# Kernel optimization log

Measured on AMD Instinct MI355X. Metric: run time of the kernel, lower is better.

## Reference

```python
import jax, jax.numpy as jnp
import numpy as np

B, S_LONG, S_SHORT, C_IN, H, D_STATE = 16384, 100, 10, 4, 64, 16
BN_EPS = 1e-5


def setup_inputs() -> dict:
    key = jax.random.key(0)
    ks = jax.random.split(key, 32)
    n = lambda i, shape, s=0.1: (jax.random.normal(ks[i], shape, dtype=jnp.float32) * s)
    inp = {
        "x": jax.random.normal(ks[0], (B, S_LONG, C_IN), dtype=jnp.float32),
        # ConvolutionalEyes (Conv1d weights are [out, in, k])
        "conv1_w": n(1, (H, C_IN, 3)), "conv1_b": n(2, (H,)),
        "conv2_w": n(3, (H, H, 5)),    "conv2_b": n(4, (H,)),
        "conv3_w": n(5, (H, H, 7)),    "conv3_b": n(6, (H,)),
        # BatchNorm1d (eval mode: running_mean=0, running_var=1)
        "bn1_g": jnp.ones((H,)), "bn1_b": jnp.zeros((H,)),
        "bn2_g": jnp.ones((H,)), "bn2_b": jnp.zeros((H,)),
        "bn3_g": jnp.ones((H,)), "bn3_b": jnp.zeros((H,)),
        # input_proj
        "proj_w": n(7, (C_IN, H)), "proj_b": n(8, (H,)),
        # MambaBlock (proj_in exists in torch code but is unused in forward)
        "A": n(9, (D_STATE, D_STATE)),
        "Bm": n(10, (H, D_STATE)),
        "Cm": n(11, (D_STATE, H)),
        "out_w": n(12, (H, H)), "out_b": n(13, (H,)),
        # ContextualGate
        "g1_w": n(14, (2 * H, H)), "g1_b": n(15, (H,)),
        "g2_w": n(16, (H, H)),     "g2_b": n(17, (H,)),
        # trading head
        "h1_w": n(18, (H, 32)), "h1_b": n(19, (32,)),
        "h2_w": n(20, (32, 3)), "h2_b": n(21, (3,)),
    }
    return inp


def _conv_bn_relu(x, w, b, g, beta, pad):
    # x: [B, C, L], w: [O, I, K]
    y = jax.lax.conv_general_dilated(x, w, (1,), [(pad, pad)],
                                     dimension_numbers=("NCW", "OIW", "NCW"))
    y = y + b[None, :, None]
    # eval-mode BN with running_mean=0, running_var=1
    y = g[None, :, None] * y * jax.lax.rsqrt(jnp.float32(1.0 + BN_EPS)) + beta[None, :, None]
    return jax.nn.relu(y)


def reference(x, conv1_w, conv1_b, conv2_w, conv2_b, conv3_w, conv3_b,
              bn1_g, bn1_b, bn2_g, bn2_b, bn3_g, bn3_b,
              proj_w, proj_b, A, Bm, Cm, out_w, out_b,
              g1_w, g1_b, g2_w, g2_b, h1_w, h1_b, h2_w, h2_b):
    # --- split windows ---
    x_short = x[:, -S_SHORT:, :]          # [B, 10, 4]
    x_long = x                            # [B, 100, 4]

    # --- ConvolutionalEyes (dropout = identity in eval) ---
    xc = jnp.swapaxes(x_short, 1, 2)      # [B, 4, 10]
    xc = _conv_bn_relu(xc, conv1_w, conv1_b, bn1_g, bn1_b, 1)
    xc = _conv_bn_relu(xc, conv2_w, conv2_b, bn2_g, bn2_b, 2)
    xc = _conv_bn_relu(xc, conv3_w, conv3_b, bn3_g, bn3_b, 3)
    short_features = jnp.mean(xc, axis=2)  # [B, 64]

    # --- input projection ---
    xp = x_long @ proj_w + proj_b          # [B, 100, 64]

    # --- MambaBlock: sequential scan over time ---
    def step(h, x_t):                      # h: [B, 16], x_t: [B, 64]
        h = jnp.tanh(x_t @ Bm + h @ A.T)
        return h, h @ Cm                   # y_t: [B, 64]

    h0 = jnp.zeros((x.shape[0], D_STATE), dtype=x.dtype)
    _, ys = jax.lax.scan(step, h0, jnp.swapaxes(xp, 0, 1))  # ys: [100, B, 64]
    long_context = ys[-1] @ out_w + out_b  # proj_out applied, last timestep

    # --- ContextualGate ---
    combined = jnp.concatenate([short_features, long_context], axis=1)  # [B, 128]
    gate = jax.nn.sigmoid(jnp.tanh(combined @ g1_w + g1_b) @ g2_w + g2_b)
    filtered = short_features * gate

    # --- trading head (dropout = identity in eval) ---
    logits = jax.nn.relu(filtered @ h1_w + h1_b) @ h2_w + h2_b  # [B, 3]
    return logits
```

## Files before the change

### kernel.cpp

```cpp
#include <hip/hip_runtime.h>
#include <cstddef>

#define NB 16384
#define ITER 4
#define TS 720
#define NRNN (NB/128)

typedef __attribute__((ext_vector_type(8))) _Float16 half8;
typedef __attribute__((ext_vector_type(4))) _Float16 half4;
typedef __attribute__((ext_vector_type(4))) float f32x4;
typedef __attribute__((ext_vector_type(2))) float f32x2;
typedef __attribute__((ext_vector_type(16))) float f32x16;

#define OFF_W1T 0
#define OFF_SC1 768
#define OFF_SH1 832
#define OFF_SC2 896
#define OFF_SH2 960
#define OFF_SC3 1024
#define OFF_SH3 1088
#define OFF_PB  1152
#define OFF_PBB 1216
#define OFF_W2H 2304
#define OFF_W2L 12544
#define OFF_W3H 22784
#define OFF_W3L 37120
#define OFF_SF  51456
#define OFF_H   (51456 + NB*64)
#define OFF_TF  1362176
#define OFF_A2  1378048
#define WS_NEED ((size_t)11863808 * 4)

#define G1H 0
#define G1L 8192
#define G2H 16384
#define G2L 20480
#define H1H 24576
#define H1L 26624
#define H2H 28672
#define H2L 29184
#define COH 29696
#define COL 30720
#define TFH 31744

static __device__ __forceinline__ f32x16 mfma32(half8 a, half8 b, f32x16 c) {
  return __builtin_amdgcn_mfma_f32_32x32x16_f16(a, b, c, 0, 0, 0);
}
static __device__ __forceinline__ f32x4 mfma16(half4 a, half4 b, f32x4 c) {
  return __builtin_amdgcn_mfma_f32_16x16x16f16(a, b, c, 0, 0, 0);
}
static __device__ __forceinline__ f32x4 mfma16k32(half8 a, half8 b, f32x4 c) {
  return __builtin_amdgcn_mfma_f32_16x16x32_f16(a, b, c, 0, 0, 0);
}

__global__ __launch_bounds__(256) void prep_kernel(
    const float* __restrict__ conv1_w, const float* __restrict__ conv1_b,
    const float* __restrict__ conv2_w, const float* __restrict__ conv2_b,
    const float* __restrict__ conv3_w, const float* __restrict__ conv3_b,
    const float* __restrict__ bn1_g, const float* __restrict__ bn1_b,
    const float* __restrict__ bn2_g, const float* __restrict__ bn2_b,
    const float* __restrict__ bn3_g, const float* __restrict__ bn3_b,
    const float* __restrict__ proj_w, const float* __restrict__ proj_b,
    const float* __restrict__ A, const float* __restrict__ Bm,
    const float* __restrict__ Cm, const float* __restrict__ out_w,
    const float* __restrict__ g1_w, const float* __restrict__ g2_w,
    const float* __restrict__ h1_w, const float* __restrict__ h2_w,
    float* __restrict__ ws)
{
  int tid = blockIdx.x * blockDim.x + threadIdx.x;
  int nt = gridDim.x * blockDim.x;
  const float s = rsqrtf(1.0f + 1e-5f);

  for (int i = tid; i < 64*12; i += nt) {
    int o = i & 63, rk = i >> 6;
    ws[OFF_W1T + i] = conv1_w[o*12 + rk];
  }
  for (int o = tid; o < 64; o += nt) {
    float s1 = bn1_g[o]*s, s2 = bn2_g[o]*s, s3 = bn3_g[o]*s;
    ws[OFF_SC1+o] = s1; ws[OFF_SH1+o] = s1*conv1_b[o] + bn1_b[o];
    ws[OFF_SC2+o] = s2; ws[OFF_SH2+o] = s2*conv2_b[o] + bn2_b[o];
    ws[OFF_SC3+o] = s3; ws[OFF_SH3+o] = s3*conv3_b[o] + bn3_b[o];
  }
  {
    _Float16* w2h = (_Float16*)(ws + OFF_W2H);
    _Float16* w2l = (_Float16*)(ws + OFF_W2L);
    for (int i = tid; i < 20*2*64; i += nt) {
      int lane = i & 63, ot = (i >> 6) & 1, sk = i >> 7;
      int tap = sk >> 2, ic0 = (sk & 3)*16 + (lane >> 5)*8;
      int o = ot*32 + (lane & 31);
      #pragma unroll
      for (int j = 0; j < 8; ++j) {
        float w = conv2_w[o*320 + (ic0 + j)*5 + tap];
        _Float16 hi = (_Float16)w;
        w2h[(size_t)i*8 + j] = hi;
        w2l[(size_t)i*8 + j] = (_Float16)(w - (float)hi);
      }
    }
  }
  {
    _Float16* w3h = (_Float16*)(ws + OFF_W3H);
    _Float16* w3l = (_Float16*)(ws + OFF_W3L);
    for (int i = tid; i < 28*2*64; i += nt) {
      int lane = i & 63, ot = (i >> 6) & 1, sk = i >> 7;
      int tap = sk >> 2, ic0 = (sk & 3)*16 + (lane >> 5)*8;
      int o = ot*32 + (lane & 31);
      #pragma unroll
      for (int j = 0; j < 8; ++j) {
        float w = conv3_w[o*448 + (ic0 + j)*7 + tap];
        _Float16 hi = (_Float16)w;
        w3h[(size_t)i*8 + j] = hi;
        w3l[(size_t)i*8 + j] = (_Float16)(w - (float)hi);
      }
    }
  }
  for (int i = tid; i < 64; i += nt) {
    int c = i >> 4, j = i & 15;
    float acc = 0.f;
    for (int m = 0; m < 64; ++m) acc += proj_w[c*64+m]*Bm[m*16+j];
    ws[OFF_PB + i] = acc;
  }
  for (int j = tid; j < 16; j += nt) {
    float acc = 0.f;
    for (int m = 0; m < 64; ++m) acc += proj_b[m]*Bm[m*16+j];
    ws[OFF_PBB + j] = acc;
  }

  _Float16* tf = (_Float16*)(ws + OFF_TF);
  for (int i = tid; i < 16*64; i += nt) {
    int l = i & 63, f = i >> 6, mt = f >> 2, ks = f & 3;
    int o = mt*16 + (l & 15), kb = ks*32 + (l >> 4)*8;
    #pragma unroll
    for (int j = 0; j < 8; ++j) {
      float w = g1_w[(size_t)(kb + j)*64 + o];
      _Float16 hi = (_Float16)w;
      tf[G1H + (size_t)i*8 + j] = hi;
      tf[G1L + (size_t)i*8 + j] = (_Float16)(w - (float)hi);
    }
  }
  for (int i = tid; i < 8*64; i += nt) {
    int l = i & 63, f = i >> 6, mt = f >> 1, ks = f & 1;
    int o = mt*16 + (l & 15), kb = ks*32 + (l >> 4)*8;
    #pragma unroll
    for (int j = 0; j < 8; ++j) {
      float w = g2_w[(size_t)(kb + j)*64 + o];
      _Float16 hi = (_Float16)w;
      tf[G2H + (size_t)i*8 + j] = hi;
      tf[G2L + (size_t)i*8 + j] = (_Float16)(w - (float)hi);
    }
  }
  for (int i = tid; i < 4*64; i += nt) {
    int l = i & 63, f = i >> 6, mt = f >> 1, ks = f & 1;
    int hx = mt*16 + (l & 15), kb = ks*32 + (l >> 4)*8;
    #pragma unroll
    for (int j = 0; j < 8; ++j) {
      float w = h1_w[(size_t)(kb + j)*32 + hx];
      _Float16 hi = (_Float16)w;
      tf[H1H + (size_t)i*8 + j] = hi;
      tf[H1L + (size_t)i*8 + j] = (_Float16)(w - (float)hi);
    }
  }
  for (int i = tid; i < 64; i += nt) {
    int l = i, m = l & 15, kb = (l >> 4)*8;
    #pragma unroll
    for (int j = 0; j < 8; ++j) {
      float w = (m < 3) ? h2_w[(size_t)(kb + j)*3 + m] : 0.f;
      _Float16 hi = (_Float16)w;
      tf[H2H + (size_t)i*8 + j] = hi;
      tf[H2L + (size_t)i*8 + j] = (_Float16)(w - (float)hi);
    }
  }
  for (int i = tid; i < 4*64; i += nt) {
    int l = i & 63, mt = i >> 6;
    int o = mt*16 + (l & 15), kb = (l >> 4)*4;
    #pragma unroll
    for (int j = 0; j < 4; ++j) {
      float acc = 0.f;
      for (int m = 0; m < 64; ++m) acc += Cm[(kb + j)*64 + m]*out_w[m*64 + o];
      _Float16 hi = (_Float16)acc;
      tf[COH + (size_t)i*4 + j] = hi;
      tf[COL + (size_t)i*4 + j] = (_Float16)(acc - (float)hi);
    }
  }
}

__global__ __launch_bounds__(512) void conv12_kernel(
    const float* __restrict__ x, const float* __restrict__ wsr,
    _Float16* __restrict__ a2gh, _Float16* __restrict__ a2gl,
    const float* __restrict__ A, float* __restrict__ hout)
{
  __shared__ __align__(16) _Float16 sW[40960];
  __shared__ __align__(16) _Float16 a1h[16][TS], a1l[16][TS];

  const int tid = threadIdx.x;
  const int lane = tid & 63;
  const int wid = tid >> 6;

  if (blockIdx.x < NRNN) {
    const int colb = lane & 15;
    const int q = lane >> 4;
    const size_t b = ((size_t)blockIdx.x*8 + wid)*16 + colb;

    const f32x4 av = *(const f32x4*)(A + (size_t)(lane & 15)*16 + q*4);
    half4 Ahi, Alo;
    #pragma unroll
    for (int j = 0; j < 4; ++j) {
      _Float16 hi = (_Float16)av[j];
      Ahi[j] = hi;
      Alo[j] = (_Float16)(av[j] - (float)hi);
    }
    f32x4 pb0 = *(const f32x4*)(wsr + OFF_PB + 0*16 + q*4);
    f32x4 pb1 = *(const f32x4*)(wsr + OFF_PB + 1*16 + q*4);
    f32x4 pb2 = *(const f32x4*)(wsr + OFF_PB + 2*16 + q*4);
    f32x4 pb3 = *(const f32x4*)(wsr + OFF_PB + 3*16 + q*4);
    f32x4 pbb = *(const f32x4*)(wsr + OFF_PBB + q*4);

    const float* xb = x + b*400;
    half4 hh = {}, hl = {};
    f32x4 hf;
    #pragma unroll 2
    for (int t = 0; t < 100; ++t) {
      const f32x4 xv = *(const f32x4*)(xb + t*4);
      f32x4 U;
      #pragma unroll
      for (int r = 0; r < 4; ++r)
        U[r] = pbb[r] + xv[0]*pb0[r] + xv[1]*pb1[r] + xv[2]*pb2[r] + xv[3]*pb3[r];
      f32x4 u = mfma16(Alo, hh, U);
      u = mfma16(Ahi, hl, u);
      u = mfma16(Ahi, hh, u);
      #pragma unroll
      for (int r = 0; r < 4; ++r) {
        float e = __expf(2.f*u[r]);
        float hn = 1.f - 2.f/(e + 1.f);
        hf[r] = hn;
        _Float16 hi = (_Float16)hn;
        hh[r] = hi;
        hl[r] = (_Float16)(hn - (float)hi);
      }
    }
    *(f32x4*)(hout + b*16 + q*4) = hf;
    return;
  }

  const int n = lane & 15;
  const int nc = (n < 10) ? n : 9;
  const int kh8 = (lane >> 5) * 8;
  const int rq = 4 * (lane >> 5);
  const int lbL = 2*wid + ((lane >> 4) & 1);
  const half8 z8 = {};
  const size_t B0g = (size_t)(blockIdx.x - NRNN) * 16;

  {
    const f32x4* src = (const f32x4*)(wsr + OFF_W2H);
    f32x4* dst = (f32x4*)sW;
    for (int i = tid; i < 5120; i += 512) dst[i] = src[i];
  }
  {
    const float sc1 = wsr[OFF_SC1 + lane], sh1 = wsr[OFF_SH1 + lane];
    #pragma unroll
    for (int bb = 0; bb < 2; ++bb) {
      const int lb = 2*wid + bb;
      const size_t gb = B0g + lb;
      float xv[4][12];
      #pragma unroll
      for (int c = 0; c < 4; ++c) { xv[c][0] = 0.f; xv[c][11] = 0.f; }
      #pragma unroll
      for (int tt = 0; tt < 10; ++tt)
        #pragma unroll
        for (int c = 0; c < 4; ++c)
          xv[c][1 + tt] = x[gb*400 + (90 + tt)*4 + c];
      float a1[10];
      #pragma unroll
      for (int t = 0; t < 10; ++t) a1[t] = 0.f;
      #pragma unroll
      for (int c = 0; c < 4; ++c)
        #pragma unroll
        for (int k = 0; k < 3; ++k) {
          const float wv = wsr[OFF_W1T + (c*3 + k)*64 + lane];
          #pragma unroll
          for (int t = 0; t < 10; ++t) a1[t] += wv * xv[c][t + k];
        }
      #pragma unroll
      for (int t = 0; t < 10; ++t) {
        float v = sc1*a1[t] + sh1;
        v = v > 0.f ? v : 0.f;
        _Float16 hi = (_Float16)v;
        a1h[lb][t*72 + lane] = hi;
        a1l[lb][t*72 + lane] = (_Float16)(v - (float)hi);
      }
    }
  }
  __syncthreads();

  {
    f32x16 acc0, acc1;
    #pragma unroll
    for (int r = 0; r < 16; ++r) { acc0[r] = 0.f; acc1[r] = 0.f; }
    const _Float16* bhp = &a1h[lbL][0];
    const _Float16* blp = &a1l[lbL][0];
    #pragma unroll
    for (int sk = 0; sk < 20; ++sk) {
      const int tap = sk >> 2, icb = (sk & 3)*16;
      const int t = nc + tap - 2;
      const int tc = t < 0 ? 0 : (t > 9 ? 9 : t);
      const bool valid = (t >= 0) & (t <= 9);
      const int off = tc*72 + icb + kh8;
      half8 bh = *(const half8*)(bhp + off);
      half8 bl = *(const half8*)(blp + off);
      bh = valid ? bh : z8;
      bl = valid ? bl : z8;
      const half8 wh0 = *(const half8*)(sW + (size_t)(sk*2 + 0)*512 + lane*8);
      const half8 wh1 = *(const half8*)(sW + (size_t)(sk*2 + 1)*512 + lane*8);
      const half8 wl0 = *(const half8*)(sW + (size_t)(40 + sk*2)*512 + lane*8);
      const half8 wl1 = *(const half8*)(sW + (size_t)(41 + sk*2)*512 + lane*8);
      acc0 = mfma32(wh0, bh, acc0);
      acc0 = mfma32(wh0, bl, acc0);
      acc0 = mfma32(wl0, bh, acc0);
      acc1 = mfma32(wh1, bh, acc1);
      acc1 = mfma32(wh1, bl, acc1);
      acc1 = mfma32(wl1, bh, acc1);
    }
    if (n < 10) {
      const size_t gb = B0g + lbL;
      auto epi = [&](const f32x16& ac, int ot) {
        #pragma unroll
        for (int q = 0; q < 4; ++q) {
          const int rowb = 8*q + rq + ot*32;
          const f32x4 sc = *(const f32x4*)(wsr + OFF_SC2 + rowb);
          const f32x4 sh = *(const f32x4*)(wsr + OFF_SH2 + rowb);
          half4 h4, l4;
          #pragma unroll
          for (int r = 0; r < 4; ++r) {
            float v = sc[r]*ac[4*q + r] + sh[r];
            v = v > 0.f ? v : 0.f;
            _Float16 hi = (_Float16)v;
            h4[r] = hi;
            l4[r] = (_Float16)(v - (float)hi);
          }
          *(half4*)(a2gh + gb*640 + n*64 + rowb) = h4;
          *(half4*)(a2gl + gb*640 + n*64 + rowb) = l4;
        }
      };
      epi(acc0, 0);
      epi(acc1, 1);
    }
  }
}

__global__ __launch_bounds__(512) void conv3k_kernel(
    const float* __restrict__ wsr,
    const _Float16* __restrict__ a2gh, const _Float16* __restrict__ a2gl,
    float* __restrict__ sfp)
{
  __shared__ __align__(16) _Float16 sW[57344];
  __shared__ __align__(16) _Float16 a2h[16][TS], a2l[16][TS];

  const int tid = threadIdx.x;
  const int lane = tid & 63;
  const int wid = tid >> 6;
  const int n = lane & 15;
  const int nc = (n < 10) ? n : 9;
  const int kh8 = (lane >> 5) * 8;
  const int rq = 4 * (lane >> 5);
  const int lbL = 2*wid + ((lane >> 4) & 1);
  const half8 z8 = {};
  const size_t B0g = (size_t)blockIdx.x * 16;

  {
    const f32x4* src = (const f32x4*)(wsr + OFF_W3H);
    f32x4* dst = (f32x4*)sW;
    for (int i = tid; i < 7168; i += 512) dst[i] = src[i];
  }
  {
    for (int i = tid; i < 1280; i += 512) {
      int idx = i*8;
      int lb = idx / 640, rem = idx % 640;
      int t = rem >> 6, o = rem & 63;
      *(half8*)(&a2h[lb][t*72 + o]) = *(const half8*)(a2gh + (B0g + lb)*640 + rem);
      *(half8*)(&a2l[lb][t*72 + o]) = *(const half8*)(a2gl + (B0g + lb)*640 + rem);
    }
  }
  __syncthreads();

  {
    f32x16 acc0, acc1;
    #pragma unroll
    for (int r = 0; r < 16; ++r) { acc0[r] = 0.f; acc1[r] = 0.f; }
    const _Float16* bhp = &a2h[lbL][0];
    const _Float16* blp = &a2l[lbL][0];
    #pragma unroll
    for (int sk = 0; sk < 28; ++sk) {
      const int tap = sk >> 2, icb = (sk & 3)*16;
      const int t = nc + tap - 3;
      const int tc = t < 0 ? 0 : (t > 9 ? 9 : t);
      const bool valid = (t >= 0) & (t <= 9);
      const int off = tc*72 + icb + kh8;
      half8 bh = *(const half8*)(bhp + off);
      half8 bl = *(const half8*)(blp + off);
      bh = valid ? bh : z8;
      bl = valid ? bl : z8;
      const half8 wh0 = *(const half8*)(sW + (size_t)(sk*2 + 0)*512 + lane*8);
      const half8 wh1 = *(const half8*)(sW + (size_t)(sk*2 + 1)*512 + lane*8);
      const half8 wl0 = *(const half8*)(sW + (size_t)(56 + sk*2)*512 + lane*8);
      const half8 wl1 = *(const half8*)(sW + (size_t)(57 + sk*2)*512 + lane*8);
      acc0 = mfma32(wh0, bh, acc0);
      acc0 = mfma32(wh0, bl, acc0);
      acc0 = mfma32(wl0, bh, acc0);
      acc1 = mfma32(wh1, bh, acc1);
      acc1 = mfma32(wh1, bl, acc1);
      acc1 = mfma32(wl1, bh, acc1);
    }
    auto epi = [&](const f32x16& ac, int ot) {
      #pragma unroll
      for (int q = 0; q < 4; ++q) {
        const int rowb = 8*q + rq + ot*32;
        const f32x4 sc = *(const f32x4*)(wsr + OFF_SC3 + rowb);
        const f32x4 sh = *(const f32x4*)(wsr + OFF_SH3 + rowb);
        f32x4 v;
        #pragma unroll
        for (int r = 0; r < 4; ++r) {
          float t2 = sc[r]*ac[4*q + r] + sh[r];
          t2 = t2 > 0.f ? t2 : 0.f;
          v[r] = (n < 10) ? t2 : 0.f;
        }
        #pragma unroll
        for (int r = 0; r < 4; ++r) {
          v[r] += __shfl_xor(v[r], 1, 16);
          v[r] += __shfl_xor(v[r], 2, 16);
          v[r] += __shfl_xor(v[r], 4, 16);
          v[r] += __shfl_xor(v[r], 8, 16);
        }
        if (n == 0)
          *(f32x4*)(sfp + (B0g + lbL)*64 + rowb) = v * 0.1f;
      }
    };
    epi(acc0, 0);
    epi(acc1, 1);
  }
}

__global__ __launch_bounds__(256) void conv_kernel(
    const float* __restrict__ x, const float* __restrict__ wsr,
    float* __restrict__ sfp)
{
  __shared__ __align__(16) _Float16 sW[57344];
  __shared__ __align__(16) _Float16 a1h[8][TS], a1l[8][TS];
  __shared__ __align__(16) _Float16 a2h[8][TS], a2l[8][TS];

  const int tid = threadIdx.x;
  const int lane = tid & 63;
  const int wid = tid >> 6;
  const int n = lane & 15;
  const int nc = (n < 10) ? n : 9;
  const int kh8 = (lane >> 5) * 8;
  const int rq = 4 * (lane >> 5);
  const int lb0 = (wid >> 1)*4 + (wid & 1)*2;
  const int lbL = lb0 + ((lane >> 4) & 1);
  const half8 z8 = {};
  const float sc1 = wsr[OFF_SC1 + lane], sh1 = wsr[OFF_SH1 + lane];

  for (int it = 0; it < ITER; ++it) {
    const size_t gbase = (size_t)blockIdx.x*(8*ITER) + (size_t)it*8;
    {
      const f32x4* src = (const f32x4*)(wsr + OFF_W2H);
      f32x4* dst = (f32x4*)sW;
      for (int i = tid; i < 5120; i += 256) dst[i] = src[i];
    }
    #pragma unroll
    for (int bb = 0; bb < 2; ++bb) {
      const int lb = lb0 + bb;
      const size_t gb = gbase + lb;
      float xv[4][12];
      #pragma unroll
      for (int c = 0; c < 4; ++c) { xv[c][0] = 0.f; xv[c][11] = 0.f; }
      #pragma unroll
      for (int tt = 0; tt < 10; ++tt)
        #pragma unroll
        for (int c = 0; c < 4; ++c)
          xv[c][1 + tt] = x[gb*400 + (90 + tt)*4 + c];
      float a1[10];
      #pragma unroll
      for (int t = 0; t < 10; ++t) a1[t] = 0.f;
      #pragma unroll
      for (int c = 0; c < 4; ++c)
        #pragma unroll
        for (int k = 0; k < 3; ++k) {
          const float wv = wsr[OFF_W1T + (c*3 + k)*64 + lane];
          #pragma unroll
          for (int t = 0; t < 10; ++t) a1[t] += wv * xv[c][t + k];
        }
      #pragma unroll
      for (int t = 0; t < 10; ++t) {
        float v = sc1*a1[t] + sh1;
        v = v > 0.f ? v : 0.f;
        _Float16 hi = (_Float16)v;
        a1h[lb][t*72 + lane] = hi;
        a1l[lb][t*72 + lane] = (_Float16)(v - (float)hi);
      }
    }
    __syncthreads();
    {
      f32x16 acc0, acc1;
      #pragma unroll
      for (int r = 0; r < 16; ++r) { acc0[r] = 0.f; acc1[r] = 0.f; }
      const _Float16* bhp = &a1h[lbL][0];
      const _Float16* blp = &a1l[lbL][0];
      #pragma unroll
      for (int sk = 0; sk < 20; ++sk) {
        const int tap = sk >> 2, icb = (sk & 3)*16;
        const int t = nc + tap - 2;
        const int tc = t < 0 ? 0 : (t > 9 ? 9 : t);
        const bool valid = (t >= 0) & (t <= 9);
        const int off = tc*72 + icb + kh8;
        half8 bh = *(const half8*)(bhp + off);
        half8 bl = *(const half8*)(blp + off);
        bh = valid ? bh : z8;
        bl = valid ? bl : z8;
        const half8 wh0 = *(const half8*)(sW + (size_t)(sk*2 + 0)*512 + lane*8);
        const half8 wh1 = *(const half8*)(sW + (size_t)(sk*2 + 1)*512 + lane*8);
        const half8 wl0 = *(const half8*)(sW + (size_t)(40 + sk*2)*512 + lane*8);
        const half8 wl1 = *(const half8*)(sW + (size_t)(41 + sk*2)*512 + lane*8);
        acc0 = mfma32(wh0, bh, acc0);
        acc0 = mfma32(wh0, bl, acc0);
        acc0 = mfma32(wl0, bh, acc0);
        acc1 = mfma32(wh1, bh, acc1);
        acc1 = mfma32(wh1, bl, acc1);
        acc1 = mfma32(wl1, bh, acc1);
      }
      if (n < 10) {
        auto epi = [&](const f32x16& ac, int ot) {
          #pragma unroll
          for (int q = 0; q < 4; ++q) {
            const int rowb = 8*q + rq + ot*32;
            const f32x4 sc = *(const f32x4*)(wsr + OFF_SC2 + rowb);
            const f32x4 sh = *(const f32x4*)(wsr + OFF_SH2 + rowb);
            half4 h4, l4;
            #pragma unroll
            for (int r = 0; r < 4; ++r) {
              float v = sc[r]*ac[4*q + r] + sh[r];
              v = v > 0.f ? v : 0.f;
              _Float16 hi = (_Float16)v;
              h4[r] = hi;
              l4[r] = (_Float16)(v - (float)hi);
            }
            *(half4*)(&a2h[lbL][n*72 + rowb]) = h4;
            *(half4*)(&a2l[lbL][n*72 + rowb]) = l4;
          }
        };
        epi(acc0, 0);
        epi(acc1, 1);
      }
    }
    __syncthreads();
    {
      const f32x4* src = (const f32x4*)(wsr + OFF_W3H);
      f32x4* dst = (f32x4*)sW;
      for (int i = tid; i < 7168; i += 256) dst[i] = src[i];
    }
    __syncthreads();
    {
      f32x16 acc0, acc1;
      #pragma unroll
      for (int r = 0; r < 16; ++r) { acc0[r] = 0.f; acc1[r] = 0.f; }
      const _Float16* bhp = &a2h[lbL][0];
      const _Float16* blp = &a2l[lbL][0];
      #pragma unroll
      for (int sk = 0; sk < 28; ++sk) {
        const int tap = sk >> 2, icb = (sk & 3)*16;
        const int t = nc + tap - 3;
        const int tc = t < 0 ? 0 : (t > 9 ? 9 : t);
        const bool valid = (t >= 0) & (t <= 9);
        const int off = tc*72 + icb + kh8;
        half8 bh = *(const half8*)(bhp + off);
        half8 bl = *(const half8*)(blp + off);
        bh = valid ? bh : z8;
        bl = valid ? bl : z8;
        const half8 wh0 = *(const half8*)(sW + (size_t)(sk*2 + 0)*512 + lane*8);
        const half8 wh1 = *(const half8*)(sW + (size_t)(sk*2 + 1)*512 + lane*8);
        const half8 wl0 = *(const half8*)(sW + (size_t)(56 + sk*2)*512 + lane*8);
        const half8 wl1 = *(const half8*)(sW + (size_t)(57 + sk*2)*512 + lane*8);
        acc0 = mfma32(wh0, bh, acc0);
        acc0 = mfma32(wh0, bl, acc0);
        acc0 = mfma32(wl0, bh, acc0);
        acc1 = mfma32(wh1, bh, acc1);
        acc1 = mfma32(wh1, bl, acc1);
        acc1 = mfma32(wl1, bh, acc1);
      }
      auto epi = [&](const f32x16& ac, int ot) {
        #pragma unroll
        for (int q = 0; q < 4; ++q) {
          const int rowb = 8*q + rq + ot*32;
          const f32x4 sc = *(const f32x4*)(wsr + OFF_SC3 + rowb);
          const f32x4 sh = *(const f32x4*)(wsr + OFF_SH3 + rowb);
          f32x4 v;
          #pragma unroll
          for (int r = 0; r < 4; ++r) {
            float t2 = sc[r]*ac[4*q + r] + sh[r];
            t2 = t2 > 0.f ? t2 : 0.f;
            v[r] = (n < 10) ? t2 : 0.f;
          }
          #pragma unroll
          for (int r = 0; r < 4; ++r) {
            v[r] += __shfl_xor(v[r], 1, 16);
            v[r] += __shfl_xor(v[r], 2, 16);
            v[r] += __shfl_xor(v[r], 4, 16);
            v[r] += __shfl_xor(v[r], 8, 16);
          }
          if (n == 0)
            *(f32x4*)(sfp + (gbase + lbL)*64 + rowb) = v * 0.1f;
        }
      };
      epi(acc0, 0);
      epi(acc1, 1);
    }
    __syncthreads();
  }
}

__global__ __launch_bounds__(256) void rnn_kernel(
    const float* __restrict__ x, const float* __restrict__ wsr,
    const float* __restrict__ A, float* __restrict__ hout)
{
  const int lane = threadIdx.x & 63;
  const int wid = threadIdx.x >> 6;
  const int colb = lane & 15;
  const int q = lane >> 4;
  const size_t b = ((size_t)blockIdx.x*4 + wid)*16 + colb;

  const f32x4 av = *(const f32x4*)(A + (size_t)(lane & 15)*16 + q*4);
  half4 Ahi, Alo;
  #pragma unroll
  for (int j = 0; j < 4; ++j) {
    _Float16 hi = (_Float16)av[j];
    Ahi[j] = hi;
    Alo[j] = (_Float16)(av[j] - (float)hi);
  }
  f32x4 pb0 = *(const f32x4*)(wsr + OFF_PB + 0*16 + q*4);
  f32x4 pb1 = *(const f32x4*)(wsr + OFF_PB + 1*16 + q*4);
  f32x4 pb2 = *(const f32x4*)(wsr + OFF_PB + 2*16 + q*4);
  f32x4 pb3 = *(const f32x4*)(wsr + OFF_PB + 3*16 + q*4);
  f32x4 pbb = *(const f32x4*)(wsr + OFF_PBB + q*4);

  const float* xb = x + b*400;
  half4 hh = {}, hl = {};
  f32x4 hf;
  #pragma unroll 2
  for (int t = 0; t < 100; ++t) {
    const f32x4 xv = *(const f32x4*)(xb + t*4);
    f32x4 U;
    #pragma unroll
    for (int r = 0; r < 4; ++r)
      U[r] = pbb[r] + xv[0]*pb0[r] + xv[1]*pb1[r] + xv[2]*pb2[r] + xv[3]*pb3[r];
    f32x4 u = mfma16(Alo, hh, U);
    u = mfma16(Ahi, hl, u);
    u = mfma16(Ahi, hh, u);
    #pragma unroll
    for (int r = 0; r < 4; ++r) {
      float e = __expf(2.f*u[r]);
      float hn = 1.f - 2.f/(e + 1.f);
      hf[r] = hn;
      _Float16 hi = (_Float16)hn;
      hh[r] = hi;
      hl[r] = (_Float16)(hn - (float)hi);
    }
  }
  *(f32x4*)(hout + b*16 + q*4) = hf;
}

#define CMBH 0
#define CMBL 2176
#define T1H  4352
#define T1L  5504
#define FLH  6656
#define FLL  7808
#define RH   8960
#define RL   9600
__global__ __launch_bounds__(256) void tail_kernel(
    const float* __restrict__ wsr,
    const float* __restrict__ g1_b, const float* __restrict__ g2_b,
    const float* __restrict__ h1_b, const float* __restrict__ h2_b,
    const float* __restrict__ out_b, float* __restrict__ out)
{
  __shared__ __align__(16) _Float16 sWF[TFH];
  __shared__ __align__(16) _Float16 sAct[4*10240];

  const int tid = threadIdx.x;
  const int lane = tid & 63;
  const int wid = tid >> 6;
  const int n = lane & 15;
  const int q = lane >> 4;
  const int B0 = blockIdx.x*64 + wid*16;

  {
    const f32x4* src = (const f32x4*)(wsr + OFF_TF);
    f32x4* dst = (f32x4*)sWF;
    for (int i = tid; i < TFH/8; i += 256) dst[i] = src[i];
  }
  __syncthreads();

  _Float16* wa = sAct + wid*10240;
  const float* sf = wsr + OFF_SF;
  const float* hws = wsr + OFF_H;

  const f32x4 hv = *(const f32x4*)(hws + (size_t)(B0 + n)*16 + q*4);
  half4 hh, hl;
  #pragma unroll
  for (int j = 0; j < 4; ++j) {
    _Float16 hi = (_Float16)hv[j];
    hh[j] = hi;
    hl[j] = (_Float16)(hv[j] - (float)hi);
  }
  f32x4 lc[4];
  #pragma unroll
  for (int mt = 0; mt < 4; ++mt) {
    lc[mt] = *(const f32x4*)(out_b + mt*16 + q*4);
    const half4 ah = *(const half4*)(sWF + COH + (size_t)(mt*64 + lane)*4);
    const half4 al = *(const half4*)(sWF + COL + (size_t)(mt*64 + lane)*4);
    lc[mt] = mfma16(al, hh, lc[mt]);
    lc[mt] = mfma16(ah, hl, lc[mt]);
    lc[mt] = mfma16(ah, hh, lc[mt]);
  }
  f32x4 sfv[4];
  #pragma unroll
  for (int mt = 0; mt < 4; ++mt) {
    sfv[mt] = *(const f32x4*)(sf + (size_t)(B0 + n)*64 + mt*16 + q*4);
    half4 sh4, sl4, lh4, ll4;
    #pragma unroll
    for (int r = 0; r < 4; ++r) {
      _Float16 hi = (_Float16)sfv[mt][r];
      sh4[r] = hi; sl4[r] = (_Float16)(sfv[mt][r] - (float)hi);
      _Float16 hi2 = (_Float16)lc[mt][r];
      lh4[r] = hi2; ll4[r] = (_Float16)(lc[mt][r] - (float)hi2);
    }
    *(half4*)(wa + CMBH + n*136 + mt*16 + q*4) = sh4;
    *(half4*)(wa + CMBL + n*136 + mt*16 + q*4) = sl4;
    *(half4*)(wa + CMBH + n*136 + 64 + mt*16 + q*4) = lh4;
    *(half4*)(wa + CMBL + n*136 + 64 + mt*16 + q*4) = ll4;
  }
  f32x4 u1[4];
  #pragma unroll
  for (int mt = 0; mt < 4; ++mt) u1[mt] = *(const f32x4*)(g1_b + mt*16 + q*4);
  #pragma unroll
  for (int ks = 0; ks < 4; ++ks) {
    const half8 bh = *(const half8*)(wa + CMBH + n*136 + ks*32 + q*8);
    const half8 bl = *(const half8*)(wa + CMBL + n*136 + ks*32 + q*8);
    #pragma unroll
    for (int mt = 0; mt < 4; ++mt) {
      const half8 ah = *(const half8*)(sWF + G1H + (size_t)((mt*4 + ks)*64 + lane)*8);
      const half8 al = *(const half8*)(sWF + G1L + (size_t)((mt*4 + ks)*64 + lane)*8);
      u1[mt] = mfma16k32(al, bh, u1[mt]);
      u1[mt] = mfma16k32(ah, bl, u1[mt]);
      u1[mt] = mfma16k32(ah, bh, u1[mt]);
    }
  }
  #pragma unroll
  for (int mt = 0; mt < 4; ++mt) {
    half4 th4, tl4;
    #pragma unroll
    for (int r = 0; r < 4; ++r) {
      float e = __expf(2.f*u1[mt][r]);
      float t1 = 1.f - 2.f/(e + 1.f);
      _Float16 hi = (_Float16)t1;
      th4[r] = hi; tl4[r] = (_Float16)(t1 - (float)hi);
    }
    *(half4*)(wa + T1H + n*72 + mt*16 + q*4) = th4;
    *(half4*)(wa + T1L + n*72 + mt*16 + q*4) = tl4;
  }
  f32x4 u2[4];
  #pragma unroll
  for (int mt = 0; mt < 4; ++mt) u2[mt] = *(const f32x4*)(g2_b + mt*16 + q*4);
  #pragma unroll
  for (int ks = 0; ks < 2; ++ks) {
    const half8 bh = *(const half8*)(wa + T1H + n*72 + ks*32 + q*8);
    const half8 bl = *(const half8*)(wa + T1L + n*72 + ks*32 + q*8);
    #pragma unroll
    for (int mt = 0; mt < 4; ++mt) {
      const half8 ah = *(const half8*)(sWF + G2H + (size_t)((mt*2 + ks)*64 + lane)*8);
      const half8 al = *(const half8*)(sWF + G2L + (size_t)((mt*2 + ks)*64 + lane)*8);
      u2[mt] = mfma16k32(al, bh, u2[mt]);
      u2[mt] = mfma16k32(ah, bl, u2[mt]);
      u2[mt] = mfma16k32(ah, bh, u2[mt]);
    }
  }
  #pragma unroll
  for (int mt = 0; mt < 4; ++mt) {
    half4 fh4, fl4;
    #pragma unroll
    for (int r = 0; r < 4; ++r) {
      float gate = 1.f/(1.f + __expf(-u2[mt][r]));
      float f = sfv[mt][r] * gate;
      _Float16 hi = (_Float16)f;
      fh4[r] = hi; fl4[r] = (_Float16)(f - (float)hi);
    }
    *(half4*)(wa + FLH + n*72 + mt*16 + q*4) = fh4;
    *(half4*)(wa + FLL + n*72 + mt*16 + q*4) = fl4;
  }
  f32x4 u3[2];
  #pragma unroll
  for (int mt = 0; mt < 2; ++mt) u3[mt] = *(const f32x4*)(h1_b + mt*16 + q*4);
  #pragma unroll
  for (int ks = 0; ks < 2; ++ks) {
    const half8 bh = *(const half8*)(wa + FLH + n*72 + ks*32 + q*8);
    const half8 bl = *(const half8*)(wa + FLL + n*72 + ks*32 + q*8);
    #pragma unroll
    for (int mt = 0; mt < 2; ++mt) {
      const half8 ah = *(const half8*)(sWF + H1H + (size_t)((mt*2 + ks)*64 + lane)*8);
      const half8 al = *(const half8*)(sWF + H1L + (size_t)((mt*2 + ks)*64 + lane)*8);
      u3[mt] = mfma16k32(al, bh, u3[mt]);
      u3[mt] = mfma16k32(ah, bl, u3[mt]);
      u3[mt] = mfma16k32(ah, bh, u3[mt]);
    }
  }
  #pragma unroll
  for (int mt = 0; mt < 2; ++mt) {
    half4 rh4, rl4;
    #pragma unroll
    for (int r = 0; r < 4; ++r) {
      float v = fmaxf(u3[mt][r], 0.f);
      _Float16 hi = (_Float16)v;
      rh4[r] = hi; rl4[r] = (_Float16)(v - (float)hi);
    }
    *(half4*)(wa + RH + n*40 + mt*16 + q*4) = rh4;
    *(half4*)(wa + RL + n*40 + mt*16 + q*4) = rl4;
  }
  {
    f32x4 u4;
    if (q == 0) { u4[0] = h2_b[0]; u4[1] = h2_b[1]; u4[2] = h2_b[2]; u4[3] = 0.f; }
    else { u4[0] = 0.f; u4[1] = 0.f; u4[2] = 0.f; u4[3] = 0.f; }
    const half8 bh = *(const half8*)(wa + RH + n*40 + q*8);
    const half8 bl = *(const half8*)(wa + RL + n*40 + q*8);
    const half8 ah = *(const half8*)(sWF + H2H + (size_t)lane*8);
    const half8 al = *(const half8*)(sWF + H2L + (size_t)lane*8);
    u4 = mfma16k32(al, bh, u4);
    u4 = mfma16k32(ah, bl, u4);
    u4 = mfma16k32(ah, bh, u4);
    if (q == 0) {
      out[(size_t)(B0 + n)*3 + 0] = u4[0];
      out[(size_t)(B0 + n)*3 + 1] = u4[1];
      out[(size_t)(B0 + n)*3 + 2] = u4[2];
    }
  }
}

extern "C" void kernel_launch(void* const* d_in, const int* in_sizes, int n_in,
                              void* d_out, int out_size, void* d_ws, size_t ws_size,
                              hipStream_t stream) {
  const float* x       = (const float*)d_in[0];
  const float* conv1_w = (const float*)d_in[1];
  const float* conv1_b = (const float*)d_in[2];
  const float* conv2_w = (const float*)d_in[3];
  const float* conv2_b = (const float*)d_in[4];
  const float* conv3_w = (const float*)d_in[5];
  const float* conv3_b = (const float*)d_in[6];
  const float* bn1_g   = (const float*)d_in[7];
  const float* bn1_b   = (const float*)d_in[8];
  const float* bn2_g   = (const float*)d_in[9];
  const float* bn2_b   = (const float*)d_in[10];
  const float* bn3_g   = (const float*)d_in[11];
  const float* bn3_b   = (const float*)d_in[12];
  const float* proj_w  = (const float*)d_in[13];
  const float* proj_b  = (const float*)d_in[14];
  const float* A       = (const float*)d_in[15];
  const float* Bm      = (const float*)d_in[16];
  const float* Cm      = (const float*)d_in[17];
  const float* out_w   = (const float*)d_in[18];
  const float* out_b   = (const float*)d_in[19];
  const float* g1_w    = (const float*)d_in[20];
  const float* g1_b    = (const float*)d_in[21];
  const float* g2_w    = (const float*)d_in[22];
  const float* g2_b    = (const float*)d_in[23];
  const float* h1_w    = (const float*)d_in[24];
  const float* h1_b    = (const float*)d_in[25];
  const float* h2_w    = (const float*)d_in[26];
  const float* h2_b    = (const float*)d_in[27];
  float* ws = (float*)d_ws;
  float* out = (float*)d_out;

  prep_kernel<<<64, 256, 0, stream>>>(conv1_w, conv1_b, conv2_w, conv2_b,
      conv3_w, conv3_b, bn1_g, bn1_b, bn2_g, bn2_b, bn3_g, bn3_b,
      proj_w, proj_b, A, Bm, Cm, out_w, g1_w, g2_w, h1_w, h2_w, ws);

  if (ws_size >= WS_NEED) {
    _Float16* a2gh = (_Float16*)(ws + OFF_A2);
    _Float16* a2gl = a2gh + (size_t)NB*640;
    conv12_kernel<<<NRNN + NB/16, 512, 0, stream>>>(x, ws, a2gh, a2gl,
        A, ws + OFF_H);
    conv3k_kernel<<<NB/16, 512, 0, stream>>>(ws, a2gh, a2gl, ws + OFF_SF);
  } else {
    conv_kernel<<<NB/(8*ITER), 256, 0, stream>>>(x, ws, ws + OFF_SF);
    rnn_kernel<<<NB/64, 256, 0, stream>>>(x, ws, A, ws + OFF_H);
  }
  tail_kernel<<<NB/64, 256, 0, stream>>>(ws, g1_b, g2_b, h1_b, h2_b, out_b, out);
}
```

Measured before the change: 262.1 us.

## Fuse conv2 and conv3 into one kernel keeping activations in LDS

Merges the conv1/conv2 kernel and the separate conv3 kernel into one kernel. The conv2 output now stays in shared memory and is reused in place for conv3, which removes the fp16 hi/lo activation round trip through global memory and one launch. Both conv stages now read their weights straight from global memory (cached) instead of staging them in LDS. That shrinks the shared-memory footprint and, together with launch_bounds(512,4), is meant to raise occupancy. The trade-off is more global and L2 weight traffic per wave. The fallback conv/rnn path and its workspace check are removed.

```diff
diff --git a/kernel.cpp b/kernel.cpp
--- a/kernel.cpp
+++ b/kernel.cpp
@@ -2,7 +2,6 @@
 #include <cstddef>
 
 #define NB 16384
-#define ITER 4
 #define TS 720
 #define NRNN (NB/128)
 
@@ -28,8 +27,6 @@
 #define OFF_SF  51456
 #define OFF_H   (51456 + NB*64)
 #define OFF_TF  1362176
-#define OFF_A2  1378048
-#define WS_NEED ((size_t)11863808 * 4)
 
 #define G1H 0
 #define G1L 8192
@@ -183,13 +180,12 @@
   }
 }
 
-__global__ __launch_bounds__(512) void conv12_kernel(
+__global__ __launch_bounds__(512, 4) void conv123_kernel(
     const float* __restrict__ x, const float* __restrict__ wsr,
-    _Float16* __restrict__ a2gh, _Float16* __restrict__ a2gl,
-    const float* __restrict__ A, float* __restrict__ hout)
+    const float* __restrict__ A, float* __restrict__ hout,
+    float* __restrict__ sfp)
 {
-  __shared__ __align__(16) _Float16 sW[40960];
-  __shared__ __align__(16) _Float16 a1h[16][TS], a1l[16][TS];
+  __shared__ __align__(16) _Float16 ah[16][TS], al[16][TS];
 
   const int tid = threadIdx.x;
   const int lane = tid & 63;
@@ -250,11 +246,6 @@
   const size_t B0g = (size_t)(blockIdx.x - NRNN) * 16;
 
   {
-    const f32x4* src = (const f32x4*)(wsr + OFF_W2H);
-    f32x4* dst = (f32x4*)sW;
-    for (int i = tid; i < 5120; i += 512) dst[i] = src[i];
-  }
-  {
     const float sc1 = wsr[OFF_SC1 + lane], sh1 = wsr[OFF_SH1 + lane];
     #pragma unroll
     for (int bb = 0; bb < 2; ++bb) {
@@ -284,19 +275,21 @@
         float v = sc1*a1[t] + sh1;
         v = v > 0.f ? v : 0.f;
         _Float16 hi = (_Float16)v;
-        a1h[lb][t*72 + lane] = hi;
-        a1l[lb][t*72 + lane] = (_Float16)(v - (float)hi);
+        ah[lb][t*72 + lane] = hi;
+        al[lb][t*72 + lane] = (_Float16)(v - (float)hi);
       }
     }
   }
-  __syncthreads();
+
+  const _Float16* bhp = &ah[lbL][0];
+  const _Float16* blp = &al[lbL][0];
 
   {
+    const _Float16* w2h = (const _Float16*)(wsr + OFF_W2H);
+    const _Float16* w2l = (const _Float16*)(wsr + OFF_W2L);
     f32x16 acc0, acc1;
     #pragma unroll
     for (int r = 0; r < 16; ++r) { acc0[r] = 0.f; acc1[r] = 0.f; }
-    const _Float16* bhp = &a1h[lbL][0];
-    const _Float16* blp = &a1l[lbL][0];
     #pragma unroll
     for (int sk = 0; sk < 20; ++sk) {
       const int tap = sk >> 2, icb = (sk & 3)*16;
@@ -308,10 +301,10 @@
       half8 bl = *(const half8*)(blp + off);
       bh = valid ? bh : z8;
       bl = valid ? bl : z8;
-      const half8 wh0 = *(const half8*)(sW + (size_t)(sk*2 + 0)*512 + lane*8);
-      const half8 wh1 = *(const half8*)(sW + (size_t)(sk*2 + 1)*512 + lane*8);
-      const half8 wl0 = *(const half8*)(sW + (size_t)(40 + sk*2)*512 + lane*8);
-      const half8 wl1 = *(const half8*)(sW + (size_t)(41 + sk*2)*512 + lane*8);
+      const half8 wh0 = *(const half8*)(w2h + (size_t)(sk*2 + 0)*512 + lane*8);
+      const half8 wh1 = *(const half8*)(w2h + (size_t)(sk*2 + 1)*512 + lane*8);
+      const half8 wl0 = *(const half8*)(w2l + (size_t)(sk*2 + 0)*512 + lane*8);
+      const half8 wl1 = *(const half8*)(w2l + (size_t)(sk*2 + 1)*512 + lane*8);
       acc0 = mfma32(wh0, bh, acc0);
       acc0 = mfma32(wh0, bl, acc0);
       acc0 = mfma32(wl0, bh, acc0);
@@ -320,7 +313,6 @@
       acc1 = mfma32(wl1, bh, acc1);
     }
     if (n < 10) {
-      const size_t gb = B0g + lbL;
       auto epi = [&](const f32x16& ac, int ot) {
         #pragma unroll
         for (int q = 0; q < 4; ++q) {
@@ -336,57 +328,21 @@
             h4[r] = hi;
             l4[r] = (_Float16)(v - (float)hi);
           }
-          *(half4*)(a2gh + gb*640 + n*64 + rowb) = h4;
-          *(half4*)(a2gl + gb*640 + n*64 + rowb) = l4;
+          *(half4*)(&ah[lbL][n*72 + rowb]) = h4;
+          *(half4*)(&al[lbL][n*72 + rowb]) = l4;
         }
       };
       epi(acc0, 0);
       epi(acc1, 1);
     }
   }
-}
-
-__global__ __launch_bounds__(512) void conv3k_kernel(
-    const float* __restrict__ wsr,
-    const _Float16* __restrict__ a2gh, const _Float16* __restrict__ a2gl,
-    float* __restrict__ sfp)
-{
-  __shared__ __align__(16) _Float16 sW[57344];
-  __shared__ __align__(16) _Float16 a2h[16][TS], a2l[16][TS];
-
-  const int tid = threadIdx.x;
-  const int lane = tid & 63;
-  const int wid = tid >> 6;
-  const int n = lane & 15;
-  const int nc = (n < 10) ? n : 9;
-  const int kh8 = (lane >> 5) * 8;
-  const int rq = 4 * (lane >> 5);
-  const int lbL = 2*wid + ((lane >> 4) & 1);
-  const half8 z8 = {};
-  const size_t B0g = (size_t)blockIdx.x * 16;
 
   {
-    const f32x4* src = (const f32x4*)(wsr + OFF_W3H);
-    f32x4* dst = (f32x4*)sW;
-    for (int i = tid; i < 7168; i += 512) dst[i] = src[i];
-  }
-  {
-    for (int i = tid; i < 1280; i += 512) {
-      int idx = i*8;
-      int lb = idx / 640, rem = idx % 640;
-      int t = rem >> 6, o = rem & 63;
-      *(half8*)(&a2h[lb][t*72 + o]) = *(const half8*)(a2gh + (B0g + lb)*640 + rem);
-      *(half8*)(&a2l[lb][t*72 + o]) = *(const half8*)(a2gl + (B0g + lb)*640 + rem);
-    }
-  }
-  __syncthreads();
-
-  {
+    const _Float16* w3h = (const _Float16*)(wsr + OFF_W3H);
+    const _Float16* w3l = (const _Float16*)(wsr + OFF_W3L);
     f32x16 acc0, acc1;
     #pragma unroll
     for (int r = 0; r < 16; ++r) { acc0[r] = 0.f; acc1[r] = 0.f; }
-    const _Float16* bhp = &a2h[lbL][0];
-    const _Float16* blp = &a2l[lbL][0];
     #pragma unroll
     for (int sk = 0; sk < 28; ++sk) {
       const int tap = sk >> 2, icb = (sk & 3)*16;
@@ -398,10 +354,10 @@
       half8 bl = *(const half8*)(blp + off);
       bh = valid ? bh : z8;
       bl = valid ? bl : z8;
-      const half8 wh0 = *(const half8*)(sW + (size_t)(sk*2 + 0)*512 + lane*8);
-      const half8 wh1 = *(const half8*)(sW + (size_t)(sk*2 + 1)*512 + lane*8);
-      const half8 wl0 = *(const half8*)(sW + (size_t)(56 + sk*2)*512 + lane*8);
-      const half8 wl1 = *(const half8*)(sW + (size_t)(57 + sk*2)*512 + lane*8);
+      const half8 wh0 = *(const half8*)(w3h + (size_t)(sk*2 + 0)*512 + lane*8);
+      const half8 wh1 = *(const half8*)(w3h + (size_t)(sk*2 + 1)*512 + lane*8);
+      const half8 wl0 = *(const half8*)(w3l + (size_t)(sk*2 + 0)*512 + lane*8);
+      const half8 wl1 = *(const half8*)(w3l + (size_t)(sk*2 + 1)*512 + lane*8);
       acc0 = mfma32(wh0, bh, acc0);
       acc0 = mfma32(wh0, bl, acc0);
       acc0 = mfma32(wl0, bh, acc0);
@@ -436,234 +392,6 @@
     epi(acc0, 0);
     epi(acc1, 1);
   }
-}
-
-__global__ __launch_bounds__(256) void conv_kernel(
-    const float* __restrict__ x, const float* __restrict__ wsr,
-    float* __restrict__ sfp)
-{
-  __shared__ __align__(16) _Float16 sW[57344];
-  __shared__ __align__(16) _Float16 a1h[8][TS], a1l[8][TS];
-  __shared__ __align__(16) _Float16 a2h[8][TS], a2l[8][TS];
-
-  const int tid = threadIdx.x;
-  const int lane = tid & 63;
-  const int wid = tid >> 6;
-  const int n = lane & 15;
-  const int nc = (n < 10) ? n : 9;
-  const int kh8 = (lane >> 5) * 8;
-  const int rq = 4 * (lane >> 5);
-  const int lb0 = (wid >> 1)*4 + (wid & 1)*2;
-  const int lbL = lb0 + ((lane >> 4) & 1);
-  const half8 z8 = {};
-  const float sc1 = wsr[OFF_SC1 + lane], sh1 = wsr[OFF_SH1 + lane];
-
-  for (int it = 0; it < ITER; ++it) {
-    const size_t gbase = (size_t)blockIdx.x*(8*ITER) + (size_t)it*8;
-    {
-      const f32x4* src = (const f32x4*)(wsr + OFF_W2H);
-      f32x4* dst = (f32x4*)sW;
-      for (int i = tid; i < 5120; i += 256) dst[i] = src[i];
-    }
-    #pragma unroll
-    for (int bb = 0; bb < 2; ++bb) {
-      const int lb = lb0 + bb;
-      const size_t gb = gbase + lb;
-      float xv[4][12];
-      #pragma unroll
-      for (int c = 0; c < 4; ++c) { xv[c][0] = 0.f; xv[c][11] = 0.f; }
-      #pragma unroll
-      for (int tt = 0; tt < 10; ++tt)
-        #pragma unroll
-        for (int c = 0; c < 4; ++c)
-          xv[c][1 + tt] = x[gb*400 + (90 + tt)*4 + c];
-      float a1[10];
-      #pragma unroll
-      for (int t = 0; t < 10; ++t) a1[t] = 0.f;
-      #pragma unroll
-      for (int c = 0; c < 4; ++c)
-        #pragma unroll
-        for (int k = 0; k < 3; ++k) {
-          const float wv = wsr[OFF_W1T + (c*3 + k)*64 + lane];
-          #pragma unroll
-          for (int t = 0; t < 10; ++t) a1[t] += wv * xv[c][t + k];
-        }
-      #pragma unroll
-      for (int t = 0; t < 10; ++t) {
-        float v = sc1*a1[t] + sh1;
-        v = v > 0.f ? v : 0.f;
-        _Float16 hi = (_Float16)v;
-        a1h[lb][t*72 + lane] = hi;
-        a1l[lb][t*72 + lane] = (_Float16)(v - (float)hi);
-      }
-    }
-    __syncthreads();
-    {
-      f32x16 acc0, acc1;
-      #pragma unroll
-      for (int r = 0; r < 16; ++r) { acc0[r] = 0.f; acc1[r] = 0.f; }
-      const _Float16* bhp = &a1h[lbL][0];
-      const _Float16* blp = &a1l[lbL][0];
-      #pragma unroll
-      for (int sk = 0; sk < 20; ++sk) {
-        const int tap = sk >> 2, icb = (sk & 3)*16;
-        const int t = nc + tap - 2;
-        const int tc = t < 0 ? 0 : (t > 9 ? 9 : t);
-        const bool valid = (t >= 0) & (t <= 9);
-        const int off = tc*72 + icb + kh8;
-        half8 bh = *(const half8*)(bhp + off);
-        half8 bl = *(const half8*)(blp + off);
-        bh = valid ? bh : z8;
-        bl = valid ? bl : z8;
-        const half8 wh0 = *(const half8*)(sW + (size_t)(sk*2 + 0)*512 + lane*8);
-        const half8 wh1 = *(const half8*)(sW + (size_t)(sk*2 + 1)*512 + lane*8);
-        const half8 wl0 = *(const half8*)(sW + (size_t)(40 + sk*2)*512 + lane*8);
-        const half8 wl1 = *(const half8*)(sW + (size_t)(41 + sk*2)*512 + lane*8);
-        acc0 = mfma32(wh0, bh, acc0);
-        acc0 = mfma32(wh0, bl, acc0);
-        acc0 = mfma32(wl0, bh, acc0);
-        acc1 = mfma32(wh1, bh, acc1);
-        acc1 = mfma32(wh1, bl, acc1);
-        acc1 = mfma32(wl1, bh, acc1);
-      }
-      if (n < 10) {
-        auto epi = [&](const f32x16& ac, int ot) {
-          #pragma unroll
-          for (int q = 0; q < 4; ++q) {
-            const int rowb = 8*q + rq + ot*32;
-            const f32x4 sc = *(const f32x4*)(wsr + OFF_SC2 + rowb);
-            const f32x4 sh = *(const f32x4*)(wsr + OFF_SH2 + rowb);
-            half4 h4, l4;
-            #pragma unroll
-            for (int r = 0; r < 4; ++r) {
-              float v = sc[r]*ac[4*q + r] + sh[r];
-              v = v > 0.f ? v : 0.f;
-              _Float16 hi = (_Float16)v;
-              h4[r] = hi;
-              l4[r] = (_Float16)(v - (float)hi);
-            }
-            *(half4*)(&a2h[lbL][n*72 + rowb]) = h4;
-            *(half4*)(&a2l[lbL][n*72 + rowb]) = l4;
-          }
-        };
-        epi(acc0, 0);
-        epi(acc1, 1);
-      }
-    }
-    __syncthreads();
-    {
-      const f32x4* src = (const f32x4*)(wsr + OFF_W3H);
-      f32x4* dst = (f32x4*)sW;
-      for (int i = tid; i < 7168; i += 256) dst[i] = src[i];
-    }
-    __syncthreads();
-    {
-      f32x16 acc0, acc1;
-      #pragma unroll
-      for (int r = 0; r < 16; ++r) { acc0[r] = 0.f; acc1[r] = 0.f; }
-      const _Float16* bhp = &a2h[lbL][0];
-      const _Float16* blp = &a2l[lbL][0];
-      #pragma unroll
-      for (int sk = 0; sk < 28; ++sk) {
-        const int tap = sk >> 2, icb = (sk & 3)*16;
-        const int t = nc + tap - 3;
-        const int tc = t < 0 ? 0 : (t > 9 ? 9 : t);
-        const bool valid = (t >= 0) & (t <= 9);
-        const int off = tc*72 + icb + kh8;
-        half8 bh = *(const half8*)(bhp + off);
-        half8 bl = *(const half8*)(blp + off);
-        bh = valid ? bh : z8;
-        bl = valid ? bl : z8;
-        const half8 wh0 = *(const half8*)(sW + (size_t)(sk*2 + 0)*512 + lane*8);
-        const half8 wh1 = *(const half8*)(sW + (size_t)(sk*2 + 1)*512 + lane*8);
-        const half8 wl0 = *(const half8*)(sW + (size_t)(56 + sk*2)*512 + lane*8);
-        const half8 wl1 = *(const half8*)(sW + (size_t)(57 + sk*2)*512 + lane*8);
-        acc0 = mfma32(wh0, bh, acc0);
-        acc0 = mfma32(wh0, bl, acc0);
-        acc0 = mfma32(wl0, bh, acc0);
-        acc1 = mfma32(wh1, bh, acc1);
-        acc1 = mfma32(wh1, bl, acc1);
-        acc1 = mfma32(wl1, bh, acc1);
-      }
-      auto epi = [&](const f32x16& ac, int ot) {
-        #pragma unroll
-        for (int q = 0; q < 4; ++q) {
-          const int rowb = 8*q + rq + ot*32;
-          const f32x4 sc = *(const f32x4*)(wsr + OFF_SC3 + rowb);
-          const f32x4 sh = *(const f32x4*)(wsr + OFF_SH3 + rowb);
-          f32x4 v;
-          #pragma unroll
-          for (int r = 0; r < 4; ++r) {
-            float t2 = sc[r]*ac[4*q + r] + sh[r];
-            t2 = t2 > 0.f ? t2 : 0.f;
-            v[r] = (n < 10) ? t2 : 0.f;
-          }
-          #pragma unroll
-          for (int r = 0; r < 4; ++r) {
-            v[r] += __shfl_xor(v[r], 1, 16);
-            v[r] += __shfl_xor(v[r], 2, 16);
-            v[r] += __shfl_xor(v[r], 4, 16);
-            v[r] += __shfl_xor(v[r], 8, 16);
-          }
-          if (n == 0)
-            *(f32x4*)(sfp + (gbase + lbL)*64 + rowb) = v * 0.1f;
-        }
-      };
-      epi(acc0, 0);
-      epi(acc1, 1);
-    }
-    __syncthreads();
-  }
-}
-
-__global__ __launch_bounds__(256) void rnn_kernel(
-    const float* __restrict__ x, const float* __restrict__ wsr,
-    const float* __restrict__ A, float* __restrict__ hout)
-{
-  const int lane = threadIdx.x & 63;
-  const int wid = threadIdx.x >> 6;
-  const int colb = lane & 15;
-  const int q = lane >> 4;
-  const size_t b = ((size_t)blockIdx.x*4 + wid)*16 + colb;
-
-  const f32x4 av = *(const f32x4*)(A + (size_t)(lane & 15)*16 + q*4);
-  half4 Ahi, Alo;
-  #pragma unroll
-  for (int j = 0; j < 4; ++j) {
-    _Float16 hi = (_Float16)av[j];
-    Ahi[j] = hi;
-    Alo[j] = (_Float16)(av[j] - (float)hi);
-  }
-  f32x4 pb0 = *(const f32x4*)(wsr + OFF_PB + 0*16 + q*4);
-  f32x4 pb1 = *(const f32x4*)(wsr + OFF_PB + 1*16 + q*4);
-  f32x4 pb2 = *(const f32x4*)(wsr + OFF_PB + 2*16 + q*4);
-  f32x4 pb3 = *(const f32x4*)(wsr + OFF_PB + 3*16 + q*4);
-  f32x4 pbb = *(const f32x4*)(wsr + OFF_PBB + q*4);
-
-  const float* xb = x + b*400;
-  half4 hh = {}, hl = {};
-  f32x4 hf;
-  #pragma unroll 2
-  for (int t = 0; t < 100; ++t) {
-    const f32x4 xv = *(const f32x4*)(xb + t*4);
-    f32x4 U;
-    #pragma unroll
-    for (int r = 0; r < 4; ++r)
-      U[r] = pbb[r] + xv[0]*pb0[r] + xv[1]*pb1[r] + xv[2]*pb2[r] + xv[3]*pb3[r];
-    f32x4 u = mfma16(Alo, hh, U);
-    u = mfma16(Ahi, hl, u);
-    u = mfma16(Ahi, hh, u);
-    #pragma unroll
-    for (int r = 0; r < 4; ++r) {
-      float e = __expf(2.f*u[r]);
-      float hn = 1.f - 2.f/(e + 1.f);
-      hf[r] = hn;
-      _Float16 hi = (_Float16)hn;
-      hh[r] = hi;
-      hl[r] = (_Float16)(hn - (float)hi);
-    }
-  }
-  *(f32x4*)(hout + b*16 + q*4) = hf;
 }
 
 #define CMBH 0
@@ -879,15 +607,8 @@
       conv3_w, conv3_b, bn1_g, bn1_b, bn2_g, bn2_b, bn3_g, bn3_b,
       proj_w, proj_b, A, Bm, Cm, out_w, g1_w, g2_w, h1_w, h2_w, ws);
 
-  if (ws_size >= WS_NEED) {
-    _Float16* a2gh = (_Float16*)(ws + OFF_A2);
-    _Float16* a2gl = a2gh + (size_t)NB*640;
-    conv12_kernel<<<NRNN + NB/16, 512, 0, stream>>>(x, ws, a2gh, a2gl,
-        A, ws + OFF_H);
-    conv3k_kernel<<<NB/16, 512, 0, stream>>>(ws, a2gh, a2gl, ws + OFF_SF);
-  } else {
-    conv_kernel<<<NB/(8*ITER), 256, 0, stream>>>(x, ws, ws + OFF_SF);
-    rnn_kernel<<<NB/64, 256, 0, stream>>>(x, ws, A, ws + OFF_H);
-  }
+  conv123_kernel<<<NRNN + NB/16, 512, 0, stream>>>(x, ws, A, ws + OFF_H,
+      ws + OFF_SF);
+
   tail_kernel<<<NB/64, 256, 0, stream>>>(ws, g1_b, g2_b, h1_b, h2_b, out_b, out);
 }
```

New measurement: 243.6 us. -7.1%, faster.
